# Kernel tuning notes

Measured on AMD Instinct MI355X. Metric: run time of the kernel, lower is better.

The kernel has to match this reference:

```python
import jax, jax.numpy as jnp
import numpy as np

# ---- hyperparams from init_kwargs ----
WX, WY, WW, WH = 10.0, 10.0, 5.0, 5.0      # bbox_reg_weights
BBOX_XFORM_CLIP = float(np.log(1000.0 / 16.0))
SCORE_THRESH = 0.05
NMS_THRESH = 0.5
DETECTIONS_PER_IMG = 100
MIN_SIZE = 0.01


def decode_boxes(rel_codes, boxes):
    # torchvision BoxCoder.decode_single with weights (10,10,5,5)
    widths = boxes[:, 2] - boxes[:, 0]
    heights = boxes[:, 3] - boxes[:, 1]
    ctr_x = boxes[:, 0] + 0.5 * widths
    ctr_y = boxes[:, 1] + 0.5 * heights
    dx = rel_codes[:, 0] / WX
    dy = rel_codes[:, 1] / WY
    dw = jnp.minimum(rel_codes[:, 2] / WW, BBOX_XFORM_CLIP)
    dh = jnp.minimum(rel_codes[:, 3] / WH, BBOX_XFORM_CLIP)
    pcx = dx * widths + ctr_x
    pcy = dy * heights + ctr_y
    pw = jnp.exp(dw) * widths
    ph = jnp.exp(dh) * heights
    return jnp.stack([pcx - 0.5 * pw, pcy - 0.5 * ph,
                      pcx + 0.5 * pw, pcy + 0.5 * ph], axis=1)


def iou_one_vs_all(box, boxes):
    # torchvision box_iou of one box vs all boxes -> [N]
    area1 = (box[2] - box[0]) * (box[3] - box[1])
    area2 = (boxes[:, 2] - boxes[:, 0]) * (boxes[:, 3] - boxes[:, 1])
    lt = jnp.maximum(box[:2], boxes[:, :2])
    rb = jnp.minimum(box[2:], boxes[:, 2:])
    wh = jnp.clip(rb - lt, 0.0)
    inter = wh[:, 0] * wh[:, 1]
    return inter / (area1 + area2 - inter)


def postprocess(class_logits, box_regression, proposals, image_h, image_w):
    boxes = decode_boxes(box_regression, proposals)            # [N,4]
    scores = jax.nn.softmax(class_logits, axis=-1)             # [N,C]
    # clip_boxes_to_image: x in [0,W], y in [0,H]
    boxes = jnp.stack([jnp.clip(boxes[:, 0], 0.0, image_w),
                       jnp.clip(boxes[:, 1], 0.0, image_h),
                       jnp.clip(boxes[:, 2], 0.0, image_w),
                       jnp.clip(boxes[:, 3], 0.0, image_h)], axis=1)
    # top-1 class per anchor (argmax over all classes, as in the source)
    labels = jnp.argmax(scores, axis=1)                        # [N]
    top1 = jnp.take_along_axis(scores, labels[:, None], axis=1)[:, 0]
    # score threshold + remove_small_boxes -> mask instead of dynamic filter
    valid = ((top1 > SCORE_THRESH)
             & ((boxes[:, 2] - boxes[:, 0]) >= MIN_SIZE)
             & ((boxes[:, 3] - boxes[:, 1]) >= MIN_SIZE))
    masked_scores = jnp.where(valid, top1, -1.0)

    # per-class (batched) NMS: pick max-score box, suppress same-class overlaps
    def step(s, _):
        idx = jnp.argmax(s)
        best_score = s[idx]
        best_box = boxes[idx]
        best_lab = labels[idx]
        sup = (iou_one_vs_all(best_box, boxes) > NMS_THRESH) & (labels == best_lab)
        s = jnp.where(sup, -1.0, s).at[idx].set(-1.0)
        return s, (best_box, best_score, best_lab)

    _, (out_b, out_s, out_l) = jax.lax.scan(step, masked_scores, None,
                                            length=DETECTIONS_PER_IMG)
    v = out_s > 0.0                                            # pad slots -> score<=0
    out_b = jnp.where(v[:, None], out_b, 0.0)
    out_s = jnp.where(v, out_s, 0.0)
    out_l = jnp.where(v, out_l, -1)
    return out_b, out_s, out_l


def setup_inputs() -> dict:
    key = jax.random.key(0)
    k1, k2, k3, k4, k5, k6 = jax.random.split(key, 6)
    N, C = 200000, 91
    H, W = 512, 512
    class_logits = jax.random.normal(k1, (N, C), dtype=jnp.float32)
    box_regression = jax.random.normal(k2, (N, 4), dtype=jnp.float32)
    cx = jax.random.uniform(k3, (N,), dtype=jnp.float32) * W
    cy = jax.random.uniform(k4, (N,), dtype=jnp.float32) * H
    bw = jax.random.uniform(k5, (N,), dtype=jnp.float32) * 120.0 + 8.0
    bh = jax.random.uniform(k6, (N,), dtype=jnp.float32) * 120.0 + 8.0
    proposals = jnp.stack([cx - 0.5 * bw, cy - 0.5 * bh,
                           cx + 0.5 * bw, cy + 0.5 * bh], axis=1)
    return {"class_logits": class_logits, "box_regression": box_regression,
            "proposals": proposals, "image_h": H, "image_w": W}


def reference(class_logits, box_regression, proposals, image_h, image_w):
    return postprocess(class_logits, box_regression, proposals,
                       float(image_h), float(image_w))
```

## Files before the change

kernel.cpp:

```cpp
#include <hip/hip_runtime.h>

#define NBINS   1024
#define TARGETC 192
#define CAPW    256
#define DET     100
#define XCLIP   4.135166556742356f
#define CHUNK   24
#define TILE4   576
#define K1GRID  2048
#define TOPK    8
#define NKEY    (K1GRID * TOPK)
#define SCAP    128

__device__ inline float scalar_to_float(const int* p) {
  int v = *p;
  return (v >= 0 && v < (1 << 20)) ? (float)v : __int_as_float(v);
}

struct Box { float x1, y1, x2, y2; };

__device__ inline Box decode_clip(float4 r, float4 p, float W, float H) {
  float w = p.z - p.x, h = p.w - p.y;
  float cx = p.x + 0.5f * w, cy = p.y + 0.5f * h;
  float dx = r.x / 10.f, dy = r.y / 10.f;
  float dw = fminf(r.z / 5.f, XCLIP), dh = fminf(r.w / 5.f, XCLIP);
  float pcx = dx * w + cx, pcy = dy * h + cy;
  float pw = __expf(dw) * w, ph = __expf(dh) * h;
  Box b;
  b.x1 = fminf(fmaxf(pcx - 0.5f * pw, 0.f), W);
  b.y1 = fminf(fmaxf(pcy - 0.5f * ph, 0.f), H);
  b.x2 = fminf(fmaxf(pcx + 0.5f * pw, 0.f), W);
  b.y2 = fminf(fmaxf(pcy + 0.5f * ph, 0.f), H);
  return b;
}

__global__ __launch_bounds__(256) void k1_score(
    const float* __restrict__ logits, const float* __restrict__ reg,
    const float* __restrict__ prop, const int* __restrict__ ph,
    const int* __restrict__ pw, unsigned long long* __restrict__ buckets,
    int N) {
  __shared__ float4 tile[2][TILE4];
  __shared__ unsigned long long candS[SCAP];
  __shared__ int candN;
  const int t = threadIdx.x, wv = t >> 6, lane = t & 63;
  if (t == 0) candN = 0;
  const float W = scalar_to_float(pw), H = scalar_to_float(ph);
  const int nchunks = (N + CHUNK - 1) / CHUNK;

  auto stage = [&](int cc, int b) {
    const int rows = min(CHUNK, N - cc * CHUNK);
    const int nf = rows * 91, nf4 = nf >> 2;
    const float4* s4 = (const float4*)(logits + (size_t)cc * CHUNK * 91);
    float4* dst = &tile[b][0];
    #pragma unroll
    for (int k = 0; k < 3; ++k) {
      int b4 = (wv + (k << 2)) << 6;
      if (b4 < nf4) {
        int g = b4 + lane;
        if (g > nf4 - 1) g = nf4 - 1;
        __builtin_amdgcn_global_load_lds(
            (const __attribute__((address_space(1))) void*)(s4 + g),
            (__attribute__((address_space(3))) void*)(dst + b4),
            16, 0, 0);
      }
    }
    for (int i = (nf4 << 2) + t; i < nf; i += 256)
      ((float*)dst)[i] = logits[(size_t)cc * CHUNK * 91 + i];
  };

  int c = blockIdx.x;
  int cur = 0;
  if (c < nchunks) stage(c, 0);
  __syncthreads();
  while (c < nchunks) {
    const int cn = c + gridDim.x;
    if (cn < nchunks) stage(cn, cur ^ 1);
    const int rows = min(CHUNK, N - c * CHUNK);
    const int r = t >> 3, s = t & 7;
    if (r < rows) {
      const float* rowp = (const float*)&tile[cur][0] + r * 91;
      float mv = -3.402823466e38f; int mi = 1 << 20;
      float e0 = 0.f, e1 = 0.f;
      #pragma unroll
      for (int k = 0; k < 12; ++k) {
        int j = s + (k << 3);
        if (j < 91) {
          float v = rowp[j];
          float ex = __expf(v);
          if (k & 1) e1 += ex; else e0 += ex;
          if (v > mv) { mv = v; mi = j; }
        }
      }
      float e = e0 + e1;
      #pragma unroll
      for (int m = 1; m <= 4; m <<= 1) {
        float ov = __shfl_xor(mv, m, 64);
        int   oi = __shfl_xor(mi, m, 64);
        float oe = __shfl_xor(e, m, 64);
        e += oe;
        if (ov > mv || (ov == mv && oi < mi)) { mv = ov; mi = oi; }
      }
      if (s == 0) {
        float top1 = __expf(mv) / e;
        const int row = c * CHUNK + r;
        float4 rg = ((const float4*)reg)[row];
        float4 pp = ((const float4*)prop)[row];
        Box b = decode_clip(rg, pp, W, H);
        bool valid = (top1 > 0.05f) && ((b.x2 - b.x1) >= 0.01f) && ((b.y2 - b.y1) >= 0.01f);
        if (valid) {
          unsigned int low = ((0x1FFFFFFu - (unsigned int)row) << 7) |
                             (unsigned int)mi;
          unsigned long long key =
              ((unsigned long long)__float_as_uint(top1) << 32) |
              (unsigned long long)low;
          int pos = atomicAdd(&candN, 1);
          if (pos < SCAP) candS[pos] = key;
        }
      }
    }
    __syncthreads();
    cur ^= 1;
    c = cn;
  }
  __syncthreads();
  if (t < 64) {
    int nc = candN; if (nc > SCAP) nc = SCAP;
    #pragma unroll
    for (int it = 0; it < TOPK; ++it) {
      unsigned long long a = (t < nc) ? candS[t] : 0ULL;
      unsigned long long b = (t + 64 < nc) ? candS[t + 64] : 0ULL;
      unsigned long long mk = (a >= b) ? a : b;
      unsigned int src = (a >= b) ? (unsigned int)t : (unsigned int)(t + 64);
      #pragma unroll
      for (int m = 1; m < 64; m <<= 1) {
        unsigned long long ok = __shfl_xor(mk, m, 64);
        unsigned int os = __shfl_xor(src, m, 64);
        if (ok > mk) { mk = ok; src = os; }
      }
      if (t == 0) {
        buckets[(size_t)blockIdx.x * TOPK + it] = mk;
        if (mk != 0ULL) candS[src] = 0ULL;
      }
      asm volatile("s_waitcnt lgkmcnt(0)" ::: "memory");
      __builtin_amdgcn_wave_barrier();
    }
  }
}

__global__ __launch_bounds__(1024) void k2_tail(
    const unsigned long long* __restrict__ buckets,
    const float* __restrict__ reg, const float* __restrict__ prop,
    const int* __restrict__ ph, const int* __restrict__ pw,
    float* __restrict__ out, int N) {
  __shared__ unsigned int lh[NBINS];
  __shared__ unsigned long long keys[CAPW];
  __shared__ unsigned int wsum[16];
  __shared__ unsigned int wtail[16];
  __shared__ int bstar;
  __shared__ unsigned int gcnt;
  __shared__ float rx1[CAPW], ry1[CAPW], rx2[CAPW], ry2[CAPW], rsc[CAPW];
  __shared__ int rlab[CAPW];
  __shared__ unsigned int sup[CAPW * 8];
  __shared__ unsigned int rowAny[8];
  __shared__ int keepL[DET];
  __shared__ int nkS;
  const int t = threadIdx.x;
  const int lane = t & 63, w = t >> 6;
  lh[t] = 0u;
  if (t == 0) { bstar = 0; gcnt = 0u; nkS = 0; }
  __syncthreads();
  const ulonglong2* B2 = (const ulonglong2*)buckets;
  #pragma unroll
  for (int k = 0; k < NKEY / 2048; ++k) {
    ulonglong2 kk = B2[t + (k << 10)];
    if (kk.x) {
      float s = __uint_as_float((unsigned int)(kk.x >> 32));
      int bin = (int)(s * (float)NBINS);
      if (bin > NBINS - 1) bin = NBINS - 1;
      atomicAdd(&lh[bin], 1u);
    }
    if (kk.y) {
      float s = __uint_as_float((unsigned int)(kk.y >> 32));
      int bin = (int)(s * (float)NBINS);
      if (bin > NBINS - 1) bin = NBINS - 1;
      atomicAdd(&lh[bin], 1u);
    }
  }
  __syncthreads();
  const unsigned int h0 = lh[t];
  unsigned int v = h0;
  #pragma unroll
  for (int m = 1; m < 64; m <<= 1) {
    unsigned int o = __shfl_down(v, m, 64);
    if (lane + m < 64) v += o;
  }
  if (lane == 0) wsum[w] = v;
  __syncthreads();
  if (w == 0) {
    unsigned int u = (lane < 16) ? wsum[lane] : 0u;
    unsigned int inc = u;
    #pragma unroll
    for (int m = 1; m < 16; m <<= 1) {
      unsigned int o = __shfl_down(inc, m, 64);
      if (lane + m < 16) inc += o;
    }
    if (lane < 16) wtail[lane] = inc - u;
  }
  __syncthreads();
  const unsigned int St = v + wtail[w];
  const unsigned int St1 = St - h0;
  if (St >= TARGETC && St1 < TARGETC) {
    int b = (St > CAPW) ? t + 1 : t;
    if (b > NBINS - 1) b = NBINS - 1;
    bstar = b;
  }
  __syncthreads();
  const int bs = bstar;
  const float fcut = (float)bs / (float)NBINS;
  #pragma unroll
  for (int k = 0; k < NKEY / 2048; ++k) {
    ulonglong2 kk = B2[t + (k << 10)];
    #pragma unroll
    for (int e = 0; e < 2; ++e) {
      unsigned long long key = e ? kk.y : kk.x;
      if (key) {
        float s = __uint_as_float((unsigned int)(key >> 32));
        int bin = (int)(s * (float)NBINS);
        if (bin > NBINS - 1) bin = NBINS - 1;
        if (bin >= bs) {
          unsigned int pos = atomicAdd(&gcnt, 1u);
          if (pos < CAPW) keys[pos] = key;
        }
      }
    }
  }
  (void)fcut;
  __syncthreads();
  const int count = (gcnt < (unsigned int)CAPW) ? (int)gcnt : CAPW;
  const float W = scalar_to_float(pw), H = scalar_to_float(ph);
  if (t < count) {
    unsigned long long myKey = keys[t];
    int r = 0;
    for (int j = 0; j < count; ++j) r += (keys[j] > myKey) ? 1 : 0;
    unsigned int low = (unsigned int)(myKey & 0xFFFFFFFFULL);
    int lab = (int)(low & 127u);
    int idx = (int)(0x1FFFFFFu - (low >> 7));
    if (idx < 0) idx = 0;
    if (idx > N - 1) idx = N - 1;
    float4 rr = ((const float4*)reg)[idx];
    float4 pp = ((const float4*)prop)[idx];
    Box b = decode_clip(rr, pp, W, H);
    rx1[r] = b.x1; ry1[r] = b.y1; rx2[r] = b.x2; ry2[r] = b.y2;
    rsc[r] = __uint_as_float((unsigned int)(myKey >> 32));
    rlab[r] = lab;
  }
  sup[t] = 0u; sup[t + 1024] = 0u;
  if (t < 8) rowAny[t] = 0u;
  __syncthreads();
  for (int p = t; p < (count << 8); p += 1024) {
    int a = p >> 8, b = p & 255;
    if (a < b && b < count && rlab[a] == rlab[b]) {
      float ax = fmaxf(rx1[a], rx1[b]), ay = fmaxf(ry1[a], ry1[b]);
      float bx = fminf(rx2[a], rx2[b]), by = fminf(ry2[a], ry2[b]);
      float iw = fmaxf(bx - ax, 0.f), ih = fmaxf(by - ay, 0.f);
      float inter = iw * ih;
      float a1 = (rx2[a] - rx1[a]) * (ry2[a] - ry1[a]);
      float a2 = (rx2[b] - rx1[b]) * (ry2[b] - ry1[b]);
      if (inter / (a1 + a2 - inter) > 0.5f) {
        atomicOr(&sup[a * 8 + (b >> 5)], 1u << (b & 31));
        atomicOr(&rowAny[a >> 5], 1u << (a & 31));
      }
    }
  }
  __syncthreads();
  if (t == 0) {
    unsigned int m0 = 0, m1 = 0, m2 = 0, m3 = 0, m4 = 0, m5 = 0, m6 = 0, m7 = 0;
    int nk = 0;
#define RESOLVE_WORD(WI, MREG)                                          \
    if (nk < DET && (WI) * 32 < count) {                                \
      unsigned int anyw = rowAny[WI];                                   \
      int lim = count - (WI) * 32; if (lim > 32) lim = 32;              \
      for (int b = 0; b < lim; ++b) {                                   \
        if (nk >= DET) break;                                           \
        if (!((MREG >> b) & 1u)) {                                      \
          int p = (WI) * 32 + b;                                        \
          keepL[nk++] = p;                                              \
          if ((anyw >> b) & 1u) {                                       \
            const unsigned int* row = &sup[p * 8];                      \
            m0 |= row[0]; m1 |= row[1]; m2 |= row[2]; m3 |= row[3];     \
            m4 |= row[4]; m5 |= row[5]; m6 |= row[6]; m7 |= row[7];     \
          }                                                             \
        }                                                               \
      }                                                                 \
    }
    RESOLVE_WORD(0, m0)
    RESOLVE_WORD(1, m1)
    RESOLVE_WORD(2, m2)
    RESOLVE_WORD(3, m3)
    RESOLVE_WORD(4, m4)
    RESOLVE_WORD(5, m5)
    RESOLVE_WORD(6, m6)
    RESOLVE_WORD(7, m7)
#undef RESOLVE_WORD
    nkS = nk;
  }
  __syncthreads();
  if (t < DET) {
    int nk = nkS;
    bool vld = t < nk;
    int p = vld ? keepL[t] : 0;
    out[t * 4 + 0] = vld ? rx1[p] : 0.f;
    out[t * 4 + 1] = vld ? ry1[p] : 0.f;
    out[t * 4 + 2] = vld ? rx2[p] : 0.f;
    out[t * 4 + 3] = vld ? ry2[p] : 0.f;
    out[400 + t] = vld ? rsc[p] : 0.f;
    out[500 + t] = vld ? (float)rlab[p] : -1.f;
  }
}

extern "C" void kernel_launch(void* const* d_in, const int* in_sizes, int n_in,
                              void* d_out, int out_size, void* d_ws, size_t ws_size,
                              hipStream_t stream) {
  const float* logits = (const float*)d_in[0];
  const float* reg    = (const float*)d_in[1];
  const float* prop   = (const float*)d_in[2];
  const int*   ph     = (const int*)d_in[3];
  const int*   pw     = (const int*)d_in[4];
  float* out = (float*)d_out;

  const int N = in_sizes[1] / 4;

  unsigned long long* buckets = (unsigned long long*)d_ws;

  k1_score<<<K1GRID, 256, 0, stream>>>(logits, reg, prop, ph, pw, buckets, N);
  k2_tail<<<1, 1024, 0, stream>>>(buckets, reg, prop, ph, pw, out, N);
}
```

Measured before the change: 52.88 us.

## Replace serial per-block top-K extraction with rank-based selection and privatize histogram

In the scoring kernel, the iterative wave-shuffle argmax loop over TOPK rounds is replaced by a parallel rank computation: each of 128 candidate threads counts larger keys and writes itself to bucket slot r if r < TOPK. The tail kernel splits the histogram into four copies to reduce LDS atomic contention, loads the bucket keys into registers once and reuses them for the second pass, and runs rank and NMS loops over a fixed CAPW bound with padded sentinel entries, which allows unrolling. Padding costs extra IoU work when count is small.

```diff
diff --git a/kernel.cpp b/kernel.cpp
--- a/kernel.cpp
+++ b/kernel.cpp
@@ -44,6 +44,7 @@
   __shared__ int candN;
   const int t = threadIdx.x, wv = t >> 6, lane = t & 63;
   if (t == 0) candN = 0;
+  if (t < SCAP) candS[t] = 0ULL;
   const float W = scalar_to_float(pw), H = scalar_to_float(ph);
   const int nchunks = (N + CHUNK - 1) / CHUNK;
 
@@ -123,26 +124,15 @@
     c = cn;
   }
   __syncthreads();
-  if (t < 64) {
-    int nc = candN; if (nc > SCAP) nc = SCAP;
-    #pragma unroll
-    for (int it = 0; it < TOPK; ++it) {
-      unsigned long long a = (t < nc) ? candS[t] : 0ULL;
-      unsigned long long b = (t + 64 < nc) ? candS[t + 64] : 0ULL;
-      unsigned long long mk = (a >= b) ? a : b;
-      unsigned int src = (a >= b) ? (unsigned int)t : (unsigned int)(t + 64);
-      #pragma unroll
-      for (int m = 1; m < 64; m <<= 1) {
-        unsigned long long ok = __shfl_xor(mk, m, 64);
-        unsigned int os = __shfl_xor(src, m, 64);
-        if (ok > mk) { mk = ok; src = os; }
-      }
-      if (t == 0) {
-        buckets[(size_t)blockIdx.x * TOPK + it] = mk;
-        if (mk != 0ULL) candS[src] = 0ULL;
-      }
-      asm volatile("s_waitcnt lgkmcnt(0)" ::: "memory");
-      __builtin_amdgcn_wave_barrier();
+  if (t < TOPK) buckets[(size_t)blockIdx.x * TOPK + t] = 0ULL;
+  __syncthreads();
+  if (t < SCAP) {
+    unsigned long long my = candS[t];
+    if (my != 0ULL) {
+      int r = 0;
+      #pragma unroll 8
+      for (int j = 0; j < SCAP; ++j) r += (candS[j] > my) ? 1 : 0;
+      if (r < TOPK) buckets[(size_t)blockIdx.x * TOPK + r] = my;
     }
   }
 }
@@ -152,7 +142,7 @@
     const float* __restrict__ reg, const float* __restrict__ prop,
     const int* __restrict__ ph, const int* __restrict__ pw,
     float* __restrict__ out, int N) {
-  __shared__ unsigned int lh[NBINS];
+  __shared__ unsigned int lh[4][NBINS];
   __shared__ unsigned long long keys[CAPW];
   __shared__ unsigned int wsum[16];
   __shared__ unsigned int wtail[16];
@@ -166,28 +156,32 @@
   __shared__ int nkS;
   const int t = threadIdx.x;
   const int lane = t & 63, w = t >> 6;
-  lh[t] = 0u;
+  for (int i = t; i < 4 * NBINS; i += 1024) ((unsigned int*)lh)[i] = 0u;
+  if (t < CAPW) keys[t] = 0ULL;
   if (t == 0) { bstar = 0; gcnt = 0u; nkS = 0; }
   __syncthreads();
   const ulonglong2* B2 = (const ulonglong2*)buckets;
+  ulonglong2 v8[8];
   #pragma unroll
-  for (int k = 0; k < NKEY / 2048; ++k) {
-    ulonglong2 kk = B2[t + (k << 10)];
-    if (kk.x) {
-      float s = __uint_as_float((unsigned int)(kk.x >> 32));
-      int bin = (int)(s * (float)NBINS);
-      if (bin > NBINS - 1) bin = NBINS - 1;
-      atomicAdd(&lh[bin], 1u);
-    }
-    if (kk.y) {
-      float s = __uint_as_float((unsigned int)(kk.y >> 32));
-      int bin = (int)(s * (float)NBINS);
-      if (bin > NBINS - 1) bin = NBINS - 1;
-      atomicAdd(&lh[bin], 1u);
-    }
-  }
-  __syncthreads();
-  const unsigned int h0 = lh[t];
+  for (int i = 0; i < 8; ++i) v8[i] = B2[t + (i << 10)];
+  const int sh = t & 3;
+  #pragma unroll
+  for (int i = 0; i < 8; ++i) {
+    if (v8[i].x) {
+      float s = __uint_as_float((unsigned int)(v8[i].x >> 32));
+      int b = (int)(s * (float)NBINS);
+      if (b > NBINS - 1) b = NBINS - 1;
+      atomicAdd(&lh[sh][b], 1u);
+    }
+    if (v8[i].y) {
+      float s = __uint_as_float((unsigned int)(v8[i].y >> 32));
+      int b = (int)(s * (float)NBINS);
+      if (b > NBINS - 1) b = NBINS - 1;
+      atomicAdd(&lh[sh][b], 1u);
+    }
+  }
+  __syncthreads();
+  const unsigned int h0 = lh[0][t] + lh[1][t] + lh[2][t] + lh[3][t];
   unsigned int v = h0;
   #pragma unroll
   for (int m = 1; m < 64; m <<= 1) {
@@ -216,50 +210,54 @@
   }
   __syncthreads();
   const int bs = bstar;
-  const float fcut = (float)bs / (float)NBINS;
   #pragma unroll
-  for (int k = 0; k < NKEY / 2048; ++k) {
-    ulonglong2 kk = B2[t + (k << 10)];
+  for (int i = 0; i < 8; ++i) {
     #pragma unroll
     for (int e = 0; e < 2; ++e) {
-      unsigned long long key = e ? kk.y : kk.x;
+      unsigned long long key = e ? v8[i].y : v8[i].x;
       if (key) {
         float s = __uint_as_float((unsigned int)(key >> 32));
-        int bin = (int)(s * (float)NBINS);
-        if (bin > NBINS - 1) bin = NBINS - 1;
-        if (bin >= bs) {
+        int b = (int)(s * (float)NBINS);
+        if (b > NBINS - 1) b = NBINS - 1;
+        if (b >= bs) {
           unsigned int pos = atomicAdd(&gcnt, 1u);
           if (pos < CAPW) keys[pos] = key;
         }
       }
     }
   }
-  (void)fcut;
   __syncthreads();
   const int count = (gcnt < (unsigned int)CAPW) ? (int)gcnt : CAPW;
   const float W = scalar_to_float(pw), H = scalar_to_float(ph);
-  if (t < count) {
-    unsigned long long myKey = keys[t];
+  if (t < CAPW) {
+    unsigned long long my = keys[t];
     int r = 0;
-    for (int j = 0; j < count; ++j) r += (keys[j] > myKey) ? 1 : 0;
-    unsigned int low = (unsigned int)(myKey & 0xFFFFFFFFULL);
-    int lab = (int)(low & 127u);
-    int idx = (int)(0x1FFFFFFu - (low >> 7));
-    if (idx < 0) idx = 0;
-    if (idx > N - 1) idx = N - 1;
-    float4 rr = ((const float4*)reg)[idx];
-    float4 pp = ((const float4*)prop)[idx];
-    Box b = decode_clip(rr, pp, W, H);
-    rx1[r] = b.x1; ry1[r] = b.y1; rx2[r] = b.x2; ry2[r] = b.y2;
-    rsc[r] = __uint_as_float((unsigned int)(myKey >> 32));
-    rlab[r] = lab;
+    #pragma unroll 8
+    for (int j = 0; j < CAPW; ++j) r += (keys[j] > my) ? 1 : 0;
+    if (t < count) {
+      unsigned int low = (unsigned int)(my & 0xFFFFFFFFULL);
+      int lab = (int)(low & 127u);
+      int idx = (int)(0x1FFFFFFu - (low >> 7));
+      if (idx < 0) idx = 0;
+      if (idx > N - 1) idx = N - 1;
+      float4 rr = ((const float4*)reg)[idx];
+      float4 pp = ((const float4*)prop)[idx];
+      Box b = decode_clip(rr, pp, W, H);
+      rx1[r] = b.x1; ry1[r] = b.y1; rx2[r] = b.x2; ry2[r] = b.y2;
+      rsc[r] = __uint_as_float((unsigned int)(my >> 32));
+      rlab[r] = lab;
+    } else {
+      rlab[t] = -1 - t;
+      rx1[t] = 0.f; ry1[t] = 0.f; rx2[t] = 0.f; ry2[t] = 0.f; rsc[t] = 0.f;
+    }
   }
   sup[t] = 0u; sup[t + 1024] = 0u;
   if (t < 8) rowAny[t] = 0u;
   __syncthreads();
-  for (int p = t; p < (count << 8); p += 1024) {
+  #pragma unroll 4
+  for (int p = t; p < (CAPW << 8); p += 1024) {
     int a = p >> 8, b = p & 255;
-    if (a < b && b < count && rlab[a] == rlab[b]) {
+    if (a < b && rlab[a] == rlab[b]) {
       float ax = fmaxf(rx1[a], rx1[b]), ay = fmaxf(ry1[a], ry1[b]);
       float bx = fminf(rx2[a], rx2[b]), by = fminf(ry2[a], ry2[b]);
       float iw = fmaxf(bx - ax, 0.f), ih = fmaxf(by - ay, 0.f);
```

Result: no change. 52.23 us (-1.2%).
